# Performance work log

Measured on AMD Instinct MI355X. Metric: run time of the kernel, lower is better.

Reference implementation:

```python
import jax, jax.numpy as jnp
import numpy as np

B, P, K, H, W = 32, 8, 17, 192, 192
ALPHA = 0.5
TEMP = 2.0
SIGMA = 3.0


def _bce_with_logits_mean(x, t):
    # numerically stable BCEWithLogitsLoss, reduction='mean'
    return jnp.mean(jnp.maximum(x, 0.0) - x * t + jnp.log1p(jnp.exp(-jnp.abs(x))))


def _kl_batchmean(s_logprob, t_prob):
    # torch KLDivLoss(reduction='batchmean'): sum(t * (log t - log s)) / batch
    return jnp.sum(t_prob * (jnp.log(t_prob) - s_logprob)) / s_logprob.shape[0]


def _keypoints_loss(pred, kps, vis):
    # pred: [B,K,H,W]; kps: [B,P,K,2] normalized; vis: [B,P,K] int
    b, k, h, w = pred.shape
    x = jnp.floor(kps[..., 0] * (w - 1))  # [B,P,K]; coords>=0 so floor == int()
    y = jnp.floor(kps[..., 1] * (h - 1))
    valid = ((vis > 0) & (x >= 0) & (x < w) & (y >= 0) & (y < h)).astype(pred.dtype)
    inv2s2 = 1.0 / (2.0 * SIGMA * SIGMA)
    ax = jnp.arange(w, dtype=pred.dtype)
    ay = jnp.arange(h, dtype=pred.dtype)
    # separable Gaussian: exp(-((a-x)^2+(b-y)^2)/2s^2) = gx(a)*gy(b)
    gx = jnp.exp(-(ax - x[..., None]) ** 2 * inv2s2) * valid[..., None]  # [B,P,K,W]
    gy = jnp.exp(-(ay - y[..., None]) ** 2 * inv2s2)                     # [B,P,K,H]
    # original indexes target[k][a,b] with a over grid_x (W axis); H==W required
    target = jnp.einsum('bpkw,bpkh->bkwh', gx, gy)  # [B,K,W,H] == [B,K,H,W]
    per = jnp.sum((pred - target) ** 2, axis=(1, 2, 3))          # F.mse_loss sum
    denom = jnp.sum(vis, axis=(1, 2)).astype(pred.dtype) + 1e-6
    return jnp.mean(per / denom)


def setup_inputs() -> dict:
    key = jax.random.key(0)
    k1, k2, k3, k4, k5, k6, k7 = jax.random.split(key, 7)
    return {
        's_seg_logits': jax.random.normal(k1, (B, 1, H, W), dtype=jnp.float32),
        's_pose_logits': jax.random.normal(k2, (B, K, H, W), dtype=jnp.float32),
        't_seg_logits': jax.random.normal(k3, (B, 1, H, W), dtype=jnp.float32),
        't_pose_logits': jax.random.normal(k4, (B, K, H, W), dtype=jnp.float32),
        'mask': jax.random.uniform(k5, (B, H, W), dtype=jnp.float32),
        'keypoints': jax.random.uniform(k6, (B, P, K, 2), dtype=jnp.float32),
        'visibilities': jax.random.randint(k7, (B, P, K), 0, 2, dtype=jnp.int32),
    }


def reference(s_seg_logits, s_pose_logits, t_seg_logits, t_pose_logits, mask, keypoints, visibilities):
    # task losses
    task_seg = _bce_with_logits_mean(s_seg_logits, mask[:, None])  # unsqueeze(1)
    task_pose = _keypoints_loss(s_pose_logits, keypoints, visibilities)
    task_loss = task_seg + task_pose
    # segmentation distillation (softmax over channel dim)
    s_seg_lp = jax.nn.log_softmax(s_seg_logits / TEMP, axis=1)
    t_seg_p = jax.nn.softmax(t_seg_logits / TEMP, axis=1)
    seg_distill = _kl_batchmean(s_seg_lp, t_seg_p) * TEMP ** 2
    # pose distillation (softmax over flattened K*H*W)
    s_pose_lp = jax.nn.log_softmax(s_pose_logits.reshape(s_pose_logits.shape[0], -1) / TEMP, axis=1)
    t_pose_p = jax.nn.softmax(t_pose_logits.reshape(t_pose_logits.shape[0], -1) / TEMP, axis=1)
    pose_distill = _kl_batchmean(s_pose_lp, t_pose_p) * TEMP ** 2
    distill_loss = seg_distill + pose_distill
    total = ALPHA * distill_loss + (1.0 - ALPHA) * task_loss
    return total
```

## Files before the change

kernel.cpp:

```cpp
#include <hip/hip_runtime.h>
#include <math.h>

#define B_   32
#define P_   8
#define K_   17
#define H_   192
#define W_   192
#define HW_  (H_*W_)
#define PB4   156672
#define NBLKS 2048
#define PER_B_BLKS 64
#define CHUNK 16384
#define FULL_IT 9
#define REM4  9216
#define BCE4  294912

#define STAMP_UNITS (B_*K_*P_)
#define TSQ_UNITS   (B_*K_)
#define RADIUS 18

#define WS_BLK   0
#define WS_STAMP 16384
#define WS_TSQ   20736

__device__ inline float wave_red_sum(float v) {
    for (int o = 32; o; o >>= 1) v += __shfl_xor(v, o, 64);
    return v;
}

__device__ inline void kl_elem(float sv, float tv,
        float& S2, float& Zu, float& Zv, float& A) {
    S2 += sv*sv;
    float u = tv*0.5f, v = sv*0.5f;
    float eu = __expf(u);
    Zu += eu;
    A  += eu*(u - v);
    Zv += __expf(v);
}

__global__ void __launch_bounds__(256) main_kernel(
        const float* __restrict__ s_pose, const float* __restrict__ t_pose,
        const float* __restrict__ kps,    const int* __restrict__ vis,
        const float* __restrict__ s_seg,  const float* __restrict__ mask,
        float* __restrict__ ws) {
    __shared__ float sred[4][5];
    __shared__ float gx_s[40], gy_s[40];

    const int blk = blockIdx.x;
    const int tid = threadIdx.x;
    const float inv18 = 1.0f / 18.0f;

    const int b  = blk >> 6;
    const int lg = ((blk & 63) << 8) | tid;
    const float4* s4 = (const float4*)s_pose + (size_t)b*PB4 + lg;
    const float4* t4 = (const float4*)t_pose + (size_t)b*PB4 + lg;

    float S2 = 0.f, Zu = 0.f, Zv = 0.f, A = 0.f;
#pragma unroll 3
    for (int j = 0; j < FULL_IT; j++) {
        float4 sv = s4[(size_t)j*CHUNK];
        float4 tv = t4[(size_t)j*CHUNK];
        kl_elem(sv.x, tv.x, S2, Zu, Zv, A);
        kl_elem(sv.y, tv.y, S2, Zu, Zv, A);
        kl_elem(sv.z, tv.z, S2, Zu, Zv, A);
        kl_elem(sv.w, tv.w, S2, Zu, Zv, A);
    }
    if (lg < REM4) {
        float4 sv = s4[(size_t)FULL_IT*CHUNK];
        float4 tv = t4[(size_t)FULL_IT*CHUNK];
        kl_elem(sv.x, tv.x, S2, Zu, Zv, A);
        kl_elem(sv.y, tv.y, S2, Zu, Zv, A);
        kl_elem(sv.z, tv.z, S2, Zu, Zv, A);
        kl_elem(sv.w, tv.w, S2, Zu, Zv, A);
    }

    float bce = 0.f;
    {
        int gid = (blk << 8) | tid;
        if (gid < BCE4) {
            float4 xv = ((const float4*)s_seg)[gid];
            float4 mv = ((const float4*)mask)[gid];
            bce += fmaxf(xv.x, 0.f) - xv.x*mv.x + log1pf(__expf(-fabsf(xv.x)));
            bce += fmaxf(xv.y, 0.f) - xv.y*mv.y + log1pf(__expf(-fabsf(xv.y)));
            bce += fmaxf(xv.z, 0.f) - xv.z*mv.z + log1pf(__expf(-fabsf(xv.z)));
            bce += fmaxf(xv.w, 0.f) - xv.w*mv.w + log1pf(__expf(-fabsf(xv.w)));
        }
    }

    S2  = wave_red_sum(S2);
    Zu  = wave_red_sum(Zu);
    Zv  = wave_red_sum(Zv);
    A   = wave_red_sum(A);
    bce = wave_red_sum(bce);
    {
        int w = tid >> 6;
        if ((tid & 63) == 0) {
            sred[w][0] = S2; sred[w][1] = Zu; sred[w][2] = Zv;
            sred[w][3] = A;  sred[w][4] = bce;
        }
    }
    __syncthreads();
    if (tid == 0) {
        float* o = ws + WS_BLK + (size_t)blk * 8;
#pragma unroll
        for (int c = 0; c < 5; c++)
            o[c] = sred[0][c] + sred[1][c] + sred[2][c] + sred[3][c];
    }

    for (int u = blk; u < STAMP_UNITS; u += NBLKS) {
        __syncthreads();
        int bb  = u / (K_*P_);
        int rem = u - bb*(K_*P_);
        int kk  = rem / P_;
        int pp  = rem - kk*P_;
        float kx = kps[((bb*P_ + pp)*K_ + kk)*2 + 0];
        float ky = kps[((bb*P_ + pp)*K_ + kk)*2 + 1];
        int   vv = vis[(bb*P_ + pp)*K_ + kk];
        float fx = floorf(kx * 191.f);
        float fy = floorf(ky * 191.f);
        bool ok = (vv > 0) && fx >= 0.f && fx < 192.f && fy >= 0.f && fy < 192.f;
        float acc = 0.f;
        if (ok) {
            int X0 = max(0, (int)fx - RADIUS), X1 = min(H_-1, (int)fx + RADIUS);
            int Y0 = max(0, (int)fy - RADIUS), Y1 = min(W_-1, (int)fy + RADIUS);
            int nr = X1 - X0 + 1, nc = Y1 - Y0 + 1;
            if (tid < nr) {
                float d = (float)(X0 + tid) - fx;
                gx_s[tid] = __expf(-d*d*inv18);
            } else if (tid >= 64 && tid - 64 < nc) {
                float d = (float)(Y0 + tid - 64) - fy;
                gy_s[tid - 64] = __expf(-d*d*inv18);
            }
            __syncthreads();
            const float* pb = s_pose + (size_t)(bb*K_ + kk) * HW_;
            int lim = nr << 6;
            for (int e = tid; e < lim; e += 256) {
                int row = e >> 6, col = e & 63;
                if (col < nc)
                    acc += pb[(X0 + row)*W_ + (Y0 + col)] * gx_s[row] * gy_s[col];
            }
        }
        acc = wave_red_sum(acc);
        if ((tid & 63) == 0) sred[tid >> 6][0] = acc;
        __syncthreads();
        if (tid == 0)
            ws[WS_STAMP + u] = sred[0][0] + sred[1][0] + sred[2][0] + sred[3][0];
    }

    if (blk < TSQ_UNITS) {
        __syncthreads();
        int bb = blk / K_, kk = blk - bb*K_;
        int pq = tid >> 2, p = pq >> 3, q = pq & 7, ln = tid & 3;
        float kxp = kps[((bb*P_ + p)*K_ + kk)*2 + 0];
        float kyp = kps[((bb*P_ + p)*K_ + kk)*2 + 1];
        float kxq = kps[((bb*P_ + q)*K_ + kk)*2 + 0];
        float kyq = kps[((bb*P_ + q)*K_ + kk)*2 + 1];
        int vp = vis[(bb*P_ + p)*K_ + kk];
        int vq = vis[(bb*P_ + q)*K_ + kk];
        float axp = floorf(kxp * 191.f), ayp = floorf(kyp * 191.f);
        float axq = floorf(kxq * 191.f), ayq = floorf(kyq * 191.f);
        bool okp = (vp > 0) && axp >= 0.f && axp < 192.f && ayp >= 0.f && ayp < 192.f;
        bool okq = (vq > 0) && axq >= 0.f && axq < 192.f && ayq >= 0.f && ayq < 192.f;
        float sx = 0.f, sy = 0.f;
        int i0 = ln * 48;
        for (int i = i0; i < i0 + 48; i++) {
            float da = (float)i - axp, db = (float)i - axq;
            sx += __expf(-(da*da + db*db)*inv18);
            float ea = (float)i - ayp, eb = (float)i - ayq;
            sy += __expf(-(ea*ea + eb*eb)*inv18);
        }
        sx += __shfl_xor(sx, 1, 64); sy += __shfl_xor(sy, 1, 64);
        sx += __shfl_xor(sx, 2, 64); sy += __shfl_xor(sy, 2, 64);
        float val = (ln == 0 && okp && okq) ? sx * sy : 0.f;
        val = wave_red_sum(val);
        if ((tid & 63) == 0) sred[tid >> 6][0] = val;
        __syncthreads();
        if (tid == 0)
            ws[WS_TSQ + blk] = sred[0][0] + sred[1][0] + sred[2][0] + sred[3][0];
    }
}

__global__ void __launch_bounds__(256) finalize_kernel(
        const float* __restrict__ ws, const int* __restrict__ vis,
        float* __restrict__ out) {
    __shared__ float rS2[B_][8], rZu[B_][8], rZv[B_][8], rA[B_][8];
    __shared__ float rCr[B_][8], rTq[B_][8];
    __shared__ int   rVs[B_][8];
    __shared__ float skl[B_], skp[B_];
    __shared__ float bw[4];
    int tid = threadIdx.x;
    int b = tid >> 3, s = tid & 7;

    float S2 = 0.f, Zu = 0.f, Zv = 0.f, A = 0.f, cr = 0.f, tq = 0.f;
    for (int j = s; j < PER_B_BLKS; j += 8) {
        const float* p = ws + WS_BLK + (size_t)(b*PER_B_BLKS + j) * 8;
        S2 += p[0]; Zu += p[1]; Zv += p[2]; A += p[3];
    }
    for (int j = s; j < K_*P_; j += 8) cr += ws[WS_STAMP + b*(K_*P_) + j];
    for (int j = s; j < K_;    j += 8) tq += ws[WS_TSQ + b*K_ + j];
    int vs = 0;
    for (int m = s; m < P_*K_; m += 8) vs += vis[b*(P_*K_) + m];
    rS2[b][s] = S2; rZu[b][s] = Zu; rZv[b][s] = Zv; rA[b][s] = A;
    rCr[b][s] = cr; rTq[b][s] = tq; rVs[b][s] = vs;

    float bce = 0.f;
    for (int i = tid; i < NBLKS; i += 256)
        bce += ws[WS_BLK + (size_t)i * 8 + 4];
    bce = wave_red_sum(bce);
    if ((tid & 63) == 0) bw[tid >> 6] = bce;
    __syncthreads();

    if (tid < B_) {
        float tS2=0.f, tZu=0.f, tZv=0.f, tA=0.f, tCr=0.f, tTq=0.f; int tVs=0;
#pragma unroll
        for (int q2 = 0; q2 < 8; q2++) {
            tS2 += rS2[tid][q2]; tZu += rZu[tid][q2]; tZv += rZv[tid][q2];
            tA  += rA[tid][q2];  tCr += rCr[tid][q2]; tTq += rTq[tid][q2];
            tVs += rVs[tid][q2];
        }
        float mse = tS2 - 2.f*tCr + tTq;
        skl[tid] = tA/tZu + (logf(tZv) - logf(tZu));
        skp[tid] = mse / ((float)tVs + 1e-6f);
    }
    __syncthreads();

    if (tid == 0) {
        float kl = 0.f, kpv = 0.f;
        for (int i = 0; i < B_; i++) { kl += skl[i]; kpv += skp[i]; }
        float bsum = bw[0] + bw[1] + bw[2] + bw[3];
        float pose_distill = 4.0f * kl / (float)B_;
        float task_seg  = bsum / (float)(B_ * HW_);
        float task_pose = kpv / (float)B_;
        out[0] = 0.5f * pose_distill + 0.5f * (task_seg + task_pose);
    }
}

extern "C" void kernel_launch(void* const* d_in, const int* in_sizes, int n_in,
                              void* d_out, int out_size, void* d_ws, size_t ws_size,
                              hipStream_t stream) {
    const float* s_seg  = (const float*)d_in[0];
    const float* s_pose = (const float*)d_in[1];
    const float* t_pose = (const float*)d_in[3];
    const float* mask   = (const float*)d_in[4];
    const float* kps    = (const float*)d_in[5];
    const int*   vis    = (const int*)d_in[6];
    float* out = (float*)d_out;
    float* ws  = (float*)d_ws;

    main_kernel<<<NBLKS, 256, 0, stream>>>(s_pose, t_pose, kps, vis,
                                           s_seg, mask, ws);
    finalize_kernel<<<1, 256, 0, stream>>>(ws, vis, out);
}
```

Baseline: 216.0 us.

## Use nontemporal streaming loads and assign stamp units to same-batch blocks

Streaming loads of pose, segmentation and mask tensors become nontemporal builtin loads, so single-use data does not pollute the cache. Gaussian stamp work units are remapped so each block handles keypoint units of its own batch index b (j over 136 with stride 64), instead of a global stride over 4352 units. This keeps the pose data the block just streamed nearby for the stamp reads and spreads stamp work evenly across blocks. The risk is that nontemporal hints interact badly with the later stamp re-reads of s_pose, which may then miss in cache.

Measured after the change: 206.7 us. 1.04x faster.

```diff
diff --git a/kernel.cpp b/kernel.cpp
--- a/kernel.cpp
+++ b/kernel.cpp
@@ -15,13 +15,19 @@
 #define REM4  9216
 #define BCE4  294912
 
-#define STAMP_UNITS (B_*K_*P_)
+#define KPU  (K_*P_)
 #define TSQ_UNITS   (B_*K_)
 #define RADIUS 18
 
 #define WS_BLK   0
 #define WS_STAMP 16384
 #define WS_TSQ   20736
+
+typedef __attribute__((ext_vector_type(4))) float f4v;
+
+__device__ inline f4v ntload4(const float* p) {
+    return __builtin_nontemporal_load((const f4v*)p);
+}
 
 __device__ inline float wave_red_sum(float v) {
     for (int o = 32; o; o >>= 1) v += __shfl_xor(v, o, 64);
@@ -52,22 +58,22 @@
 
     const int b  = blk >> 6;
     const int lg = ((blk & 63) << 8) | tid;
-    const float4* s4 = (const float4*)s_pose + (size_t)b*PB4 + lg;
-    const float4* t4 = (const float4*)t_pose + (size_t)b*PB4 + lg;
+    const float* s4 = s_pose + ((size_t)b*PB4 + lg)*4;
+    const float* t4 = t_pose + ((size_t)b*PB4 + lg)*4;
 
     float S2 = 0.f, Zu = 0.f, Zv = 0.f, A = 0.f;
 #pragma unroll 3
     for (int j = 0; j < FULL_IT; j++) {
-        float4 sv = s4[(size_t)j*CHUNK];
-        float4 tv = t4[(size_t)j*CHUNK];
+        f4v sv = ntload4(s4 + (size_t)j*CHUNK*4);
+        f4v tv = ntload4(t4 + (size_t)j*CHUNK*4);
         kl_elem(sv.x, tv.x, S2, Zu, Zv, A);
         kl_elem(sv.y, tv.y, S2, Zu, Zv, A);
         kl_elem(sv.z, tv.z, S2, Zu, Zv, A);
         kl_elem(sv.w, tv.w, S2, Zu, Zv, A);
     }
     if (lg < REM4) {
-        float4 sv = s4[(size_t)FULL_IT*CHUNK];
-        float4 tv = t4[(size_t)FULL_IT*CHUNK];
+        f4v sv = ntload4(s4 + (size_t)FULL_IT*CHUNK*4);
+        f4v tv = ntload4(t4 + (size_t)FULL_IT*CHUNK*4);
         kl_elem(sv.x, tv.x, S2, Zu, Zv, A);
         kl_elem(sv.y, tv.y, S2, Zu, Zv, A);
         kl_elem(sv.z, tv.z, S2, Zu, Zv, A);
@@ -78,8 +84,8 @@
     {
         int gid = (blk << 8) | tid;
         if (gid < BCE4) {
-            float4 xv = ((const float4*)s_seg)[gid];
-            float4 mv = ((const float4*)mask)[gid];
+            f4v xv = ntload4(s_seg + (size_t)gid*4);
+            f4v mv = ntload4(mask  + (size_t)gid*4);
             bce += fmaxf(xv.x, 0.f) - xv.x*mv.x + log1pf(__expf(-fabsf(xv.x)));
             bce += fmaxf(xv.y, 0.f) - xv.y*mv.y + log1pf(__expf(-fabsf(xv.y)));
             bce += fmaxf(xv.z, 0.f) - xv.z*mv.z + log1pf(__expf(-fabsf(xv.z)));
@@ -107,15 +113,14 @@
             o[c] = sred[0][c] + sred[1][c] + sred[2][c] + sred[3][c];
     }
 
-    for (int u = blk; u < STAMP_UNITS; u += NBLKS) {
-        __syncthreads();
-        int bb  = u / (K_*P_);
-        int rem = u - bb*(K_*P_);
-        int kk  = rem / P_;
-        int pp  = rem - kk*P_;
-        float kx = kps[((bb*P_ + pp)*K_ + kk)*2 + 0];
-        float ky = kps[((bb*P_ + pp)*K_ + kk)*2 + 1];
-        int   vv = vis[(bb*P_ + pp)*K_ + kk];
+    for (int j = blk & 63; j < KPU; j += 64) {
+        __syncthreads();
+        int u   = b*KPU + j;
+        int kk  = j / P_;
+        int pp  = j - kk*P_;
+        float kx = kps[((b*P_ + pp)*K_ + kk)*2 + 0];
+        float ky = kps[((b*P_ + pp)*K_ + kk)*2 + 1];
+        int   vv = vis[(b*P_ + pp)*K_ + kk];
         float fx = floorf(kx * 191.f);
         float fy = floorf(ky * 191.f);
         bool ok = (vv > 0) && fx >= 0.f && fx < 192.f && fy >= 0.f && fy < 192.f;
@@ -132,7 +137,7 @@
                 gy_s[tid - 64] = __expf(-d*d*inv18);
             }
             __syncthreads();
-            const float* pb = s_pose + (size_t)(bb*K_ + kk) * HW_;
+            const float* pb = s_pose + (size_t)(b*K_ + kk) * HW_;
             int lim = nr << 6;
             for (int e = tid; e < lim; e += 256) {
                 int row = e >> 6, col = e & 63;
@@ -196,8 +201,8 @@
         const float* p = ws + WS_BLK + (size_t)(b*PER_B_BLKS + j) * 8;
         S2 += p[0]; Zu += p[1]; Zv += p[2]; A += p[3];
     }
-    for (int j = s; j < K_*P_; j += 8) cr += ws[WS_STAMP + b*(K_*P_) + j];
-    for (int j = s; j < K_;    j += 8) tq += ws[WS_TSQ + b*K_ + j];
+    for (int j = s; j < KPU; j += 8) cr += ws[WS_STAMP + b*KPU + j];
+    for (int j = s; j < K_;  j += 8) tq += ws[WS_TSQ + b*K_ + j];
     int vs = 0;
     for (int m = s; m < P_*K_; m += 8) vs += vis[b*(P_*K_) + m];
     rS2[b][s] = S2; rZu[b][s] = Zu; rZv[b][s] = Zv; rA[b][s] = A;
```
